# Kernel optimization log

Hardware: AMD Instinct MI355X
Metric: run time of the kernel (lower is better)

## Reference

```python
import jax, jax.numpy as jnp
import numpy as np

ASSIGN_RATIO = 0.1  # hard-coded inside coarsen_graph in the original
EPS_CUT = 1e-7
EPS_NORM = 1e-12  # torch F.normalize eps


def _normalize_batch_adj(adj):
    # adj: [B, N, N]
    n = adj.shape[1]
    A = adj + jnp.eye(n, dtype=adj.dtype)
    deg_inv_sqrt = jnp.clip(A.sum(-1), 1.0, None) ** -0.5  # [B, N]
    newA = deg_inv_sqrt[..., :, None] * A * deg_inv_sqrt[..., None, :]
    row_mask = (adj.sum(-1) > 0).astype(adj.dtype)  # [B, N]
    return row_mask[..., :, None] * newA


def setup_inputs():
    key = jax.random.key(0)
    k0, k1, k2, k3, k4 = jax.random.split(key, 5)
    B, N, D, T = 512, 128, 256, 512
    concept_hidden = jax.random.normal(k0, (B, N, D), jnp.float32)
    adj = jax.random.uniform(k1, (B, N, N), jnp.float32)
    head = jax.random.randint(k2, (B, T), 0, N)
    lin_w = jax.random.normal(k3, (1, D), jnp.float32) / np.sqrt(D).astype(np.float32)
    bias = jax.random.normal(k4, (1,), jnp.float32)
    return {"concept_hidden": concept_hidden, "adj": adj, "head": head,
            "lin_w": lin_w, "bias": bias}


def reference(concept_hidden, adj, head, lin_w, bias):
    # concept_hidden: [B, N, D], adj: [B, N, N], head: [B, T] node indices
    x = concept_hidden
    B, N, D = x.shape

    out = x @ lin_w.T                      # [B, N, 1]  self.lin(x)
    norm_adj = _normalize_batch_adj(adj)   # [B, N, N]
    out = norm_adj @ out + bias            # [B, N, 1]
    alpha = jax.nn.sigmoid(out ** 2)[..., 0]  # [B, N]

    # batch_num_nodes[i] = len(set(head[i]))  -> count unique via sort
    hs = jnp.sort(head, axis=-1)
    n_uniq = 1 + (hs[:, 1:] != hs[:, :-1]).sum(-1)  # [B]

    # per-sample k = ceil(n * 0.1) + 1 (only when n > 1); cut = k-th largest alpha
    k = jnp.ceil(n_uniq.astype(jnp.float32) * ASSIGN_RATIO).astype(jnp.int32) + 1
    a_desc = jnp.sort(alpha, axis=-1)[:, ::-1]       # descending
    idx = jnp.clip(k - 1, 0, N - 1)
    cut = jnp.take_along_axis(a_desc, idx[:, None], axis=-1)[:, 0]
    cut = jnp.where(n_uniq > 1, cut, jnp.zeros_like(cut))  # [B]

    cut_alpha = jax.nn.relu(alpha + EPS_CUT - cut[:, None])  # [B, N]

    # S = norm_adj * cut_alpha broadcast over rows, then L1-normalize rows
    S = norm_adj * cut_alpha[:, None, :]
    S = S / jnp.clip(jnp.abs(S).sum(-1, keepdims=True), EPS_NORM, None)

    St = jnp.swapaxes(S, 1, 2)             # [B, N, N]
    embedding_tensor = St @ x              # S^T x   [B, N, D]
    new_adj = (St @ adj) @ S               # S^T A S [B, N, N]
    return embedding_tensor, new_adj
```

## Files before the change

### kernel.cpp

```cpp
#include <hip/hip_runtime.h>

#define Bsz 512
#define Nn  128
#define Dd  256
#define Tt  512

typedef __attribute__((ext_vector_type(8))) short short8;
typedef __attribute__((ext_vector_type(4))) float f32x4;

__device__ __forceinline__ ushort f2bf(float f) {
    union { float f; unsigned u; } v; v.f = f;
    unsigned r = v.u + 0x7fffu + ((v.u >> 16) & 1u);
    return (ushort)(r >> 16);
}
__device__ __forceinline__ unsigned pk2(float a, float b) {
    return (unsigned)f2bf(a) | ((unsigned)f2bf(b) << 16);
}
__device__ __forceinline__ float bf2f(ushort u) {
    union { unsigned u; float f; } v; v.u = (unsigned)u << 16; return v.f;
}

__device__ __forceinline__ ushort* AP(ushort* base, int row, int col) {
    return base + row * 128 + (((col >> 3) ^ (row & 7)) << 3) + (col & 7);
}
__device__ __forceinline__ uint* XP(uint* base, int row, int col) {
    return base + row * 64 + (((col >> 2) ^ (row & 7)) << 2) + (col & 3);
}

__global__ __launch_bounds__(1024, 4) void mega(
    const float* __restrict__ x, const float* __restrict__ adj,
    const int* __restrict__ head, const float* __restrict__ lin_w,
    const float* __restrict__ bias,
    float* __restrict__ emb, float* __restrict__ nadj)
{
    const int t = threadIdx.x, b = blockIdx.x;
    __shared__ __align__(16) ushort adjR[Nn * 128];
    __shared__ __align__(16) ushort stR[Nn * 128];
    __shared__ __align__(16) uint   xtR0[Nn * 64];
    __shared__ __align__(16) uint   xtR1[Nn * 64];
    __shared__ float ttS[Nn], disS[Nn], maskS[Nn], alphaS[Nn], rowcS[Nn];
    __shared__ float partS[Nn][18];
    __shared__ float partS2[Nn][4];
    __shared__ int   flags[Nn];
    __shared__ int   nuniq;
    __shared__ float cutS;

    const float bias0 = bias[0];
    if (t < Nn) flags[t] = 0;
    if (t == 0) { nuniq = 0; cutS = 0.f; }

    const int lane = t & 63, w = t >> 6;
    const int l15 = lane & 15, quad = lane >> 4;
    const int mrow  = (w & 7) * 16;
    const int nhalf = (w >> 3) * 64;
    const int r = t >> 3, seg = t & 7;
    const int xrow = t & 127, kq0 = t >> 7;
    const float wv0 = lin_w[xrow], wv1 = lin_w[128 + xrow];

    int hv = 0;
    if (t < Tt) hv = head[(size_t)b * Tt + t];

    float e0[8], g0[8], e1[8], g1[8];
    {
        const float* xb = x + (size_t)b * Nn * Dd + xrow;
#pragma unroll
        for (int k = 0; k < 8; ++k) e0[k] = xb[(size_t)(8 * kq0 + k) * Dd];
#pragma unroll
        for (int k = 0; k < 8; ++k) g0[k] = xb[(size_t)(64 + 8 * kq0 + k) * Dd];
#pragma unroll
        for (int k = 0; k < 8; ++k) e1[k] = xb[(size_t)(8 * kq0 + k) * Dd + 128];
#pragma unroll
        for (int k = 0; k < 8; ++k) g1[k] = xb[(size_t)(64 + 8 * kq0 + k) * Dd + 128];
    }
    float4 av0, av1, av2, av3;
    {
        const float4* adjb = (const float4*)(adj + (size_t)b * Nn * Nn);
        av0 = adjb[t]; av1 = adjb[t + 1024]; av2 = adjb[t + 2048]; av3 = adjb[t + 3072];
    }

#pragma unroll
    for (int k = 0; k < 8; ++k) {
        float re = e0[k] * wv0 + e1[k] * wv1;
        float rg = g0[k] * wv0 + g1[k] * wv1;
        re += __shfl_xor(re, 1); re += __shfl_xor(re, 2); re += __shfl_xor(re, 4);
        rg += __shfl_xor(rg, 1); rg += __shfl_xor(rg, 2); rg += __shfl_xor(rg, 4);
        if ((lane & 7) == 0) {
            int gc = (w & 1) * 8 + (lane >> 3);
            partS[8 * kq0 + k][gc]      = re;
            partS[64 + 8 * kq0 + k][gc] = rg;
        }
    }

    {
        float s0 = av0.x + av0.y + av0.z + av0.w;
        float s1 = av1.x + av1.y + av1.z + av1.w;
        float s2 = av2.x + av2.y + av2.z + av2.w;
        float s3 = av3.x + av3.y + av3.z + av3.w;
        s0 += __shfl_xor(s0, 1); s0 += __shfl_xor(s0, 2); s0 += __shfl_xor(s0, 4);
        s1 += __shfl_xor(s1, 1); s1 += __shfl_xor(s1, 2); s1 += __shfl_xor(s1, 4);
        s2 += __shfl_xor(s2, 1); s2 += __shfl_xor(s2, 2); s2 += __shfl_xor(s2, 4);
        s3 += __shfl_xor(s3, 1); s3 += __shfl_xor(s3, 2); s3 += __shfl_xor(s3, 4);
        if ((lane & 7) == 0) {
            int q = (lane & 31) >> 3;
            int row0 = t >> 5;
            partS2[row0][q]       = s0;
            partS2[row0 + 32][q]  = s1;
            partS2[row0 + 64][q]  = s2;
            partS2[row0 + 96][q]  = s3;
        }
    }

    {
        uint4 q;
        q.x = pk2(e0[0], e0[1]); q.y = pk2(e0[2], e0[3]);
        q.z = pk2(e0[4], e0[5]); q.w = pk2(e0[6], e0[7]);
        *(uint4*)XP(xtR0, xrow, 4 * kq0) = q;
        q.x = pk2(g0[0], g0[1]); q.y = pk2(g0[2], g0[3]);
        q.z = pk2(g0[4], g0[5]); q.w = pk2(g0[6], g0[7]);
        *(uint4*)XP(xtR0, xrow, 4 * kq0 + 32) = q;
        q.x = pk2(e1[0], e1[1]); q.y = pk2(e1[2], e1[3]);
        q.z = pk2(e1[4], e1[5]); q.w = pk2(e1[6], e1[7]);
        *(uint4*)XP(xtR1, xrow, 4 * kq0) = q;
        q.x = pk2(g1[0], g1[1]); q.y = pk2(g1[2], g1[3]);
        q.z = pk2(g1[4], g1[5]); q.w = pk2(g1[6], g1[7]);
        *(uint4*)XP(xtR1, xrow, 4 * kq0 + 32) = q;
    }
    {
        float4 v; int f, rr2, c; uint2 w2;
        v = av0; f = t;        rr2 = f >> 5; c = (f & 31) * 4; w2.x = pk2(v.x, v.y); w2.y = pk2(v.z, v.w); *(uint2*)AP(adjR, rr2, c) = w2;
        v = av1; f = t + 1024; rr2 = f >> 5; c = (f & 31) * 4; w2.x = pk2(v.x, v.y); w2.y = pk2(v.z, v.w); *(uint2*)AP(adjR, rr2, c) = w2;
        v = av2; f = t + 2048; rr2 = f >> 5; c = (f & 31) * 4; w2.x = pk2(v.x, v.y); w2.y = pk2(v.z, v.w); *(uint2*)AP(adjR, rr2, c) = w2;
        v = av3; f = t + 3072; rr2 = f >> 5; c = (f & 31) * 4; w2.x = pk2(v.x, v.y); w2.y = pk2(v.z, v.w); *(uint2*)AP(adjR, rr2, c) = w2;
    }
    __syncthreads();

    if (t < Tt) flags[hv] = 1;

    {
        float d = partS[r][2 * seg] + partS[r][2 * seg + 1];
        float s = (seg < 4) ? partS2[r][seg] : 0.f;
        d += __shfl_xor(d, 1); d += __shfl_xor(d, 2); d += __shfl_xor(d, 4);
        s += __shfl_xor(s, 1); s += __shfl_xor(s, 2); s += __shfl_xor(s, 4);
        if (seg == 0) {
            maskS[r] = (s > 0.f) ? 1.f : 0.f;
            float dis = 1.f / sqrtf(fmaxf(s + 1.f, 1.f));
            disS[r] = dis;
            ttS[r]  = dis * d;
        }
    }
    __syncthreads();

    {
        short8 a0 = *(const short8*)AP(adjR, r, seg * 16);
        short8 a1 = *(const short8*)AP(adjR, r, seg * 16 + 8);
        f32x4 t0 = *(const f32x4*)&ttS[seg * 16];
        f32x4 t1 = *(const f32x4*)&ttS[seg * 16 + 4];
        f32x4 t2 = *(const f32x4*)&ttS[seg * 16 + 8];
        f32x4 t3 = *(const f32x4*)&ttS[seg * 16 + 12];
        float s = 0.f;
#pragma unroll
        for (int j = 0; j < 4; ++j) {
            s += bf2f((ushort)a0[j])     * t0[j];
            s += bf2f((ushort)a0[4 + j]) * t1[j];
            s += bf2f((ushort)a1[j])     * t2[j];
            s += bf2f((ushort)a1[4 + j]) * t3[j];
        }
        s += __shfl_xor(s, 1); s += __shfl_xor(s, 2); s += __shfl_xor(s, 4);
        if (seg == 0) {
            float o = maskS[r] * disS[r] * (s + ttS[r]) + bias0;
            alphaS[r] = 1.f / (1.f + expf(-o * o));
            atomicAdd(&nuniq, flags[r]);
        }
    }
    __syncthreads();

    {
        int nu = nuniq;
        if (nu > 1) {
            float an = alphaS[r];
            int cg = 0, ce = 0;
#pragma unroll
            for (int v = 0; v < 4; ++v) {
                f32x4 A = *(const f32x4*)&alphaS[seg * 16 + 4 * v];
#pragma unroll
                for (int j = 0; j < 4; ++j) { cg += (A[j] > an); ce += (A[j] == an); }
            }
            cg += __shfl_xor(cg, 1); cg += __shfl_xor(cg, 2); cg += __shfl_xor(cg, 4);
            ce += __shfl_xor(ce, 1); ce += __shfl_xor(ce, 2); ce += __shfl_xor(ce, 4);
            if (seg == 0) {
                int idx = (int)ceilf((float)nu * 0.1f);
                if (idx > Nn - 1) idx = Nn - 1;
                if (cg <= idx && idx < cg + ce) cutS = an;
            }
        }
    }
    __syncthreads();

    {
        const float cut = cutS;
        short8 a0 = *(const short8*)AP(adjR, r, seg * 16);
        short8 a1 = *(const short8*)AP(adjR, r, seg * 16 + 8);
        float s = 0.f;
#pragma unroll
        for (int v = 0; v < 4; ++v) {
            f32x4 A = *(const f32x4*)&alphaS[seg * 16 + 4 * v];
            f32x4 D = *(const f32x4*)&disS[seg * 16 + 4 * v];
#pragma unroll
            for (int j = 0; j < 4; ++j) {
                float u = fmaxf(A[j] + 1e-7f - cut, 0.f) * D[j];
                float av = (v < 2) ? bf2f((ushort)a0[4 * v + j])
                                   : bf2f((ushort)a1[4 * (v - 2) + j]);
                s += av * u;
            }
        }
        s += __shfl_xor(s, 1); s += __shfl_xor(s, 2); s += __shfl_xor(s, 4);
        if (seg == 0) {
            float ur   = fmaxf(alphaS[r] + 1e-7f - cut, 0.f) * disS[r];
            float rsum = maskS[r] * disS[r] * (ur + s);
            rowcS[r]   = maskS[r] * disS[r] / fmaxf(rsum, 1e-12f);
        }
    }
    __syncthreads();

    {
        const float cut = cutS;
        const int m = t & 127, sl = t >> 7, k0 = sl * 16;
        const float um = fmaxf(alphaS[m] + 1e-7f - cut, 0.f) * disS[m];
        float vv[16];
#pragma unroll
        for (int j = 0; j < 16; ++j) {
            int k = k0 + j;
            vv[j] = rowcS[k] * (bf2f(*AP(adjR, k, m)) + ((k == m) ? 1.f : 0.f)) * um;
        }
        uint4 p0, p1;
        p0.x = pk2(vv[0],  vv[1]);  p0.y = pk2(vv[2],  vv[3]);
        p0.z = pk2(vv[4],  vv[5]);  p0.w = pk2(vv[6],  vv[7]);
        p1.x = pk2(vv[8],  vv[9]);  p1.y = pk2(vv[10], vv[11]);
        p1.z = pk2(vv[12], vv[13]); p1.w = pk2(vv[14], vv[15]);
        *(uint4*)AP(stR, m, k0)     = p0;
        *(uint4*)AP(stR, m, k0 + 8) = p1;
    }
    __syncthreads();

    f32x4 acc[4];
#pragma unroll
    for (int nt = 0; nt < 4; ++nt) acc[nt] = (f32x4){0.f, 0.f, 0.f, 0.f};
#pragma unroll
    for (int k0 = 0; k0 < 128; k0 += 32) {
        short8 a0 = *(const short8*)AP(adjR, mrow + l15, k0 + quad * 8);
#pragma unroll
        for (int nt = 0; nt < 4; ++nt) {
            short8 bf = *(const short8*)AP(stR, nhalf + nt * 16 + l15, k0 + quad * 8);
            acc[nt] = __builtin_amdgcn_mfma_f32_16x16x32_bf16(a0, bf, acc[nt], 0, 0, 0);
        }
    }
    __syncthreads();

#pragma unroll
    for (int nt = 0; nt < 4; ++nt) {
        int j    = nhalf + nt * 16 + l15;
        int mcol = mrow + quad * 4;
        uint2 w2;
        w2.x = pk2(acc[nt][0], acc[nt][1]);
        w2.y = pk2(acc[nt][2], acc[nt][3]);
        *(uint2*)AP(adjR, j, mcol) = w2;
    }
    __syncthreads();

#pragma unroll
    for (int nt = 0; nt < 4; ++nt) acc[nt] = (f32x4){0.f, 0.f, 0.f, 0.f};
#pragma unroll
    for (int k0 = 0; k0 < 128; k0 += 32) {
        short8 a0 = *(const short8*)AP(stR, mrow + l15, k0 + quad * 8);
#pragma unroll
        for (int nt = 0; nt < 4; ++nt) {
            short8 bf = *(const short8*)AP(adjR, nhalf + nt * 16 + l15, k0 + quad * 8);
            acc[nt] = __builtin_amdgcn_mfma_f32_16x16x32_bf16(a0, bf, acc[nt], 0, 0, 0);
        }
    }
#pragma unroll
    for (int nt = 0; nt < 4; ++nt)
#pragma unroll
        for (int rr2 = 0; rr2 < 4; ++rr2) {
            int row = mrow + quad * 4 + rr2;
            int col = nhalf + nt * 16 + l15;
            nadj[((size_t)b * Nn + row) * Nn + col] = acc[nt][rr2];
        }

    const int dcb = (w >> 3) * 64;
    f32x4 accE[4];
#pragma unroll
    for (int nt = 0; nt < 4; ++nt) accE[nt] = (f32x4){0.f, 0.f, 0.f, 0.f};
#pragma unroll
    for (int ks = 0; ks < 4; ++ks) {
        short8 aE = *(const short8*)AP(stR, mrow + l15, ks * 32 + quad * 8);
#pragma unroll
        for (int nt = 0; nt < 4; ++nt) {
            short8 bf = *(const short8*)XP(xtR0, dcb + nt * 16 + l15, ks * 16 + quad * 4);
            accE[nt] = __builtin_amdgcn_mfma_f32_16x16x32_bf16(aE, bf, accE[nt], 0, 0, 0);
        }
    }
#pragma unroll
    for (int nt = 0; nt < 4; ++nt)
#pragma unroll
        for (int rr2 = 0; rr2 < 4; ++rr2) {
            int row = mrow + quad * 4 + rr2;
            int col = dcb + nt * 16 + l15;
            emb[((size_t)b * Nn + row) * Dd + col] = accE[nt][rr2];
        }

#pragma unroll
    for (int nt = 0; nt < 4; ++nt) accE[nt] = (f32x4){0.f, 0.f, 0.f, 0.f};
#pragma unroll
    for (int ks = 0; ks < 4; ++ks) {
        short8 aE = *(const short8*)AP(stR, mrow + l15, ks * 32 + quad * 8);
#pragma unroll
        for (int nt = 0; nt < 4; ++nt) {
            short8 bf = *(const short8*)XP(xtR1, dcb + nt * 16 + l15, ks * 16 + quad * 4);
            accE[nt] = __builtin_amdgcn_mfma_f32_16x16x32_bf16(aE, bf, accE[nt], 0, 0, 0);
        }
    }
#pragma unroll
    for (int nt = 0; nt < 4; ++nt)
#pragma unroll
        for (int rr2 = 0; rr2 < 4; ++rr2) {
            int row = mrow + quad * 4 + rr2;
            int col = 128 + dcb + nt * 16 + l15;
            emb[((size_t)b * Nn + row) * Dd + col] = accE[nt][rr2];
        }
}

extern "C" void kernel_launch(void* const* d_in, const int* in_sizes, int n_in,
                              void* d_out, int out_size, void* d_ws, size_t ws_size,
                              hipStream_t stream)
{
    const float* x     = (const float*)d_in[0];
    const float* adj   = (const float*)d_in[1];
    const int*   head  = (const int*)d_in[2];
    const float* lin_w = (const float*)d_in[3];
    const float* bias  = (const float*)d_in[4];

    float* emb  = (float*)d_out;
    float* nadj = emb + (size_t)Bsz * Nn * Dd;

    mega<<<Bsz, 1024, 0, stream>>>(x, adj, head, lin_w, bias, emb, nadj);
}
```

Baseline: 201.1 us.

## Split megakernel into scalar-chain kernel and GEMM kernel via workspace

```diff
diff --git a/kernel.cpp b/kernel.cpp
--- a/kernel.cpp
+++ b/kernel.cpp
@@ -27,10 +27,158 @@
     return base + row * 64 + (((col >> 2) ^ (row & 7)) << 2) + (col & 3);
 }
 
-__global__ __launch_bounds__(1024, 4) void mega(
+__global__ __launch_bounds__(256, 2) void chainK(
     const float* __restrict__ x, const float* __restrict__ adj,
     const int* __restrict__ head, const float* __restrict__ lin_w,
     const float* __restrict__ bias,
+    float* __restrict__ uws, float* __restrict__ rws)
+{
+    const int t = threadIdx.x, b = blockIdx.x;
+    __shared__ __align__(16) uint raw[8192];
+    __shared__ float dotS[Nn], ttS[Nn], disS[Nn], maskS[Nn], alphaS[Nn];
+    __shared__ int   flags[Nn];
+    __shared__ int   nuniq;
+    __shared__ float cutS;
+
+    float*  partx = (float*)raw;
+    ushort* adjB  = (ushort*)raw;
+
+    const float bias0 = bias[0];
+    if (t < Nn) flags[t] = 0;
+    if (t == 0) { nuniq = 0; cutS = 0.f; }
+    const int hv0 = head[(size_t)b * Tt + t];
+    const int hv1 = head[(size_t)b * Tt + 256 + t];
+
+    {
+        const int rep = t >> 6, d4 = t & 63;
+        const float4 w4 = ((const float4*)lin_w)[d4];
+        const float* xb = x + (size_t)b * Nn * Dd + 4 * d4;
+#pragma unroll
+        for (int i = 0; i < 32; ++i) {
+            int k = rep * 32 + i;
+            float4 v = *(const float4*)(xb + (size_t)k * Dd);
+            float p = v.x * w4.x + v.y * w4.y + v.z * w4.z + v.w * w4.w;
+            int gs = (d4 >> 2) ^ (k & 7);
+            partx[k * 64 + (gs << 2) + (d4 & 3)] = p;
+        }
+    }
+    __syncthreads();
+    {
+        const int k = t >> 1, h = t & 1;
+        float s = 0.f;
+#pragma unroll
+        for (int jj = 0; jj < 8; ++jj) {
+            int Gs = (h * 8 + jj) ^ (k & 7);
+            f32x4 q = *(const f32x4*)&partx[k * 64 + 4 * Gs];
+            s += q[0] + q[1] + q[2] + q[3];
+        }
+        s += __shfl_xor(s, 1);
+        if (h == 0) dotS[k] = s;
+        flags[hv0] = 1; flags[hv1] = 1;
+    }
+    __syncthreads();
+    {
+        const float* adjb = adj + (size_t)b * Nn * Nn;
+#pragma unroll
+        for (int i = 0; i < 16; ++i) {
+            int f = t + 256 * i;
+            int rr = f >> 5, c = (f & 31) * 4;
+            float4 v = *(const float4*)&adjb[(size_t)rr * Nn + c];
+            uint2 w2; w2.x = pk2(v.x, v.y); w2.y = pk2(v.z, v.w);
+            *(uint2*)AP(adjB, rr, c) = w2;
+        }
+    }
+    __syncthreads();
+
+    const int row = t >> 1, h = t & 1;
+    {
+        float s = 0.f;
+#pragma unroll
+        for (int j = 0; j < 8; ++j) {
+            short8 a = *(const short8*)AP(adjB, row, h * 64 + j * 8);
+#pragma unroll
+            for (int jj = 0; jj < 8; ++jj) s += bf2f((ushort)a[jj]);
+        }
+        s += __shfl_xor(s, 1);
+        if (h == 0) {
+            maskS[row] = (s > 0.f) ? 1.f : 0.f;
+            float dis = 1.f / sqrtf(fmaxf(s + 1.f, 1.f));
+            disS[row] = dis;
+            ttS[row]  = dis * dotS[row];
+        }
+    }
+    __syncthreads();
+    {
+        float s = 0.f;
+#pragma unroll
+        for (int j = 0; j < 8; ++j) {
+            short8 a = *(const short8*)AP(adjB, row, h * 64 + j * 8);
+            f32x4 t0 = *(const f32x4*)&ttS[h * 64 + j * 8];
+            f32x4 t1 = *(const f32x4*)&ttS[h * 64 + j * 8 + 4];
+#pragma unroll
+            for (int jj = 0; jj < 4; ++jj) {
+                s += bf2f((ushort)a[jj])     * t0[jj];
+                s += bf2f((ushort)a[4 + jj]) * t1[jj];
+            }
+        }
+        s += __shfl_xor(s, 1);
+        if (h == 0) {
+            float o = maskS[row] * disS[row] * (s + ttS[row]) + bias0;
+            alphaS[row] = 1.f / (1.f + expf(-o * o));
+            atomicAdd(&nuniq, flags[row]);
+        }
+    }
+    __syncthreads();
+    {
+        int nu = nuniq;
+        if (nu > 1) {
+            float an = alphaS[row];
+            int cg = 0, ce = 0;
+#pragma unroll
+            for (int v = 0; v < 16; ++v) {
+                f32x4 A = *(const f32x4*)&alphaS[h * 64 + 4 * v];
+#pragma unroll
+                for (int jj = 0; jj < 4; ++jj) { cg += (A[jj] > an); ce += (A[jj] == an); }
+            }
+            cg += __shfl_xor(cg, 1);
+            ce += __shfl_xor(ce, 1);
+            if (h == 0) {
+                int idx = (int)ceilf((float)nu * 0.1f);
+                if (idx > Nn - 1) idx = Nn - 1;
+                if (cg <= idx && idx < cg + ce) cutS = an;
+            }
+        }
+    }
+    __syncthreads();
+    {
+        const float cut = cutS;
+        float s = 0.f;
+#pragma unroll
+        for (int j = 0; j < 8; ++j) {
+            short8 a = *(const short8*)AP(adjB, row, h * 64 + j * 8);
+            f32x4 A0 = *(const f32x4*)&alphaS[h * 64 + j * 8];
+            f32x4 A1 = *(const f32x4*)&alphaS[h * 64 + j * 8 + 4];
+            f32x4 D0 = *(const f32x4*)&disS[h * 64 + j * 8];
+            f32x4 D1 = *(const f32x4*)&disS[h * 64 + j * 8 + 4];
+#pragma unroll
+            for (int jj = 0; jj < 4; ++jj) {
+                s += bf2f((ushort)a[jj])     * fmaxf(A0[jj] + 1e-7f - cut, 0.f) * D0[jj];
+                s += bf2f((ushort)a[4 + jj]) * fmaxf(A1[jj] + 1e-7f - cut, 0.f) * D1[jj];
+            }
+        }
+        s += __shfl_xor(s, 1);
+        if (h == 0) {
+            float ur   = fmaxf(alphaS[row] + 1e-7f - cut, 0.f) * disS[row];
+            float rsum = maskS[row] * disS[row] * (ur + s);
+            rws[(size_t)b * Nn + row] = maskS[row] * disS[row] / fmaxf(rsum, 1e-12f);
+            uws[(size_t)b * Nn + row] = ur;
+        }
+    }
+}
+
+__global__ __launch_bounds__(1024, 4) void gemmK(
+    const float* __restrict__ x, const float* __restrict__ adj,
+    const float* __restrict__ uws, const float* __restrict__ rws,
     float* __restrict__ emb, float* __restrict__ nadj)
 {
     const int t = threadIdx.x, b = blockIdx.x;
@@ -38,27 +186,16 @@
     __shared__ __align__(16) ushort stR[Nn * 128];
     __shared__ __align__(16) uint   xtR0[Nn * 64];
     __shared__ __align__(16) uint   xtR1[Nn * 64];
-    __shared__ float ttS[Nn], disS[Nn], maskS[Nn], alphaS[Nn], rowcS[Nn];
-    __shared__ float partS[Nn][18];
-    __shared__ float partS2[Nn][4];
-    __shared__ int   flags[Nn];
-    __shared__ int   nuniq;
-    __shared__ float cutS;
-
-    const float bias0 = bias[0];
-    if (t < Nn) flags[t] = 0;
-    if (t == 0) { nuniq = 0; cutS = 0.f; }
+    __shared__ float uS[Nn], rowcS[Nn];
 
     const int lane = t & 63, w = t >> 6;
     const int l15 = lane & 15, quad = lane >> 4;
     const int mrow  = (w & 7) * 16;
     const int nhalf = (w >> 3) * 64;
-    const int r = t >> 3, seg = t & 7;
     const int xrow = t & 127, kq0 = t >> 7;
-    const float wv0 = lin_w[xrow], wv1 = lin_w[128 + xrow];
-
-    int hv = 0;
-    if (t < Tt) hv = head[(size_t)b * Tt + t];
+
+    float uv = 0.f, rv = 0.f;
+    if (t < Nn) { uv = uws[(size_t)b * Nn + t]; rv = rws[(size_t)b * Nn + t]; }
 
     float e0[8], g0[8], e1[8], g1[8];
     {
@@ -77,39 +214,6 @@
         const float4* adjb = (const float4*)(adj + (size_t)b * Nn * Nn);
         av0 = adjb[t]; av1 = adjb[t + 1024]; av2 = adjb[t + 2048]; av3 = adjb[t + 3072];
     }
-
-#pragma unroll
-    for (int k = 0; k < 8; ++k) {
-        float re = e0[k] * wv0 + e1[k] * wv1;
-        float rg = g0[k] * wv0 + g1[k] * wv1;
-        re += __shfl_xor(re, 1); re += __shfl_xor(re, 2); re += __shfl_xor(re, 4);
-        rg += __shfl_xor(rg, 1); rg += __shfl_xor(rg, 2); rg += __shfl_xor(rg, 4);
-        if ((lane & 7) == 0) {
-            int gc = (w & 1) * 8 + (lane >> 3);
-            partS[8 * kq0 + k][gc]      = re;
-            partS[64 + 8 * kq0 + k][gc] = rg;
-        }
-    }
-
-    {
-        float s0 = av0.x + av0.y + av0.z + av0.w;
-        float s1 = av1.x + av1.y + av1.z + av1.w;
-        float s2 = av2.x + av2.y + av2.z + av2.w;
-        float s3 = av3.x + av3.y + av3.z + av3.w;
-        s0 += __shfl_xor(s0, 1); s0 += __shfl_xor(s0, 2); s0 += __shfl_xor(s0, 4);
-        s1 += __shfl_xor(s1, 1); s1 += __shfl_xor(s1, 2); s1 += __shfl_xor(s1, 4);
-        s2 += __shfl_xor(s2, 1); s2 += __shfl_xor(s2, 2); s2 += __shfl_xor(s2, 4);
-        s3 += __shfl_xor(s3, 1); s3 += __shfl_xor(s3, 2); s3 += __shfl_xor(s3, 4);
-        if ((lane & 7) == 0) {
-            int q = (lane & 31) >> 3;
-            int row0 = t >> 5;
-            partS2[row0][q]       = s0;
-            partS2[row0 + 32][q]  = s1;
-            partS2[row0 + 64][q]  = s2;
-            partS2[row0 + 96][q]  = s3;
-        }
-    }
-
     {
         uint4 q;
         q.x = pk2(e0[0], e0[1]); q.y = pk2(e0[2], e0[3]);
@@ -132,100 +236,12 @@
         v = av2; f = t + 2048; rr2 = f >> 5; c = (f & 31) * 4; w2.x = pk2(v.x, v.y); w2.y = pk2(v.z, v.w); *(uint2*)AP(adjR, rr2, c) = w2;
         v = av3; f = t + 3072; rr2 = f >> 5; c = (f & 31) * 4; w2.x = pk2(v.x, v.y); w2.y = pk2(v.z, v.w); *(uint2*)AP(adjR, rr2, c) = w2;
     }
-    __syncthreads();
-
-    if (t < Tt) flags[hv] = 1;
-
-    {
-        float d = partS[r][2 * seg] + partS[r][2 * seg + 1];
-        float s = (seg < 4) ? partS2[r][seg] : 0.f;
-        d += __shfl_xor(d, 1); d += __shfl_xor(d, 2); d += __shfl_xor(d, 4);
-        s += __shfl_xor(s, 1); s += __shfl_xor(s, 2); s += __shfl_xor(s, 4);
-        if (seg == 0) {
-            maskS[r] = (s > 0.f) ? 1.f : 0.f;
-            float dis = 1.f / sqrtf(fmaxf(s + 1.f, 1.f));
-            disS[r] = dis;
-            ttS[r]  = dis * d;
-        }
-    }
-    __syncthreads();
-
-    {
-        short8 a0 = *(const short8*)AP(adjR, r, seg * 16);
-        short8 a1 = *(const short8*)AP(adjR, r, seg * 16 + 8);
-        f32x4 t0 = *(const f32x4*)&ttS[seg * 16];
-        f32x4 t1 = *(const f32x4*)&ttS[seg * 16 + 4];
-        f32x4 t2 = *(const f32x4*)&ttS[seg * 16 + 8];
-        f32x4 t3 = *(const f32x4*)&ttS[seg * 16 + 12];
-        float s = 0.f;
-#pragma unroll
-        for (int j = 0; j < 4; ++j) {
-            s += bf2f((ushort)a0[j])     * t0[j];
-            s += bf2f((ushort)a0[4 + j]) * t1[j];
-            s += bf2f((ushort)a1[j])     * t2[j];
-            s += bf2f((ushort)a1[4 + j]) * t3[j];
-        }
-        s += __shfl_xor(s, 1); s += __shfl_xor(s, 2); s += __shfl_xor(s, 4);
-        if (seg == 0) {
-            float o = maskS[r] * disS[r] * (s + ttS[r]) + bias0;
-            alphaS[r] = 1.f / (1.f + expf(-o * o));
-            atomicAdd(&nuniq, flags[r]);
-        }
-    }
-    __syncthreads();
-
-    {
-        int nu = nuniq;
-        if (nu > 1) {
-            float an = alphaS[r];
-            int cg = 0, ce = 0;
-#pragma unroll
-            for (int v = 0; v < 4; ++v) {
-                f32x4 A = *(const f32x4*)&alphaS[seg * 16 + 4 * v];
-#pragma unroll
-                for (int j = 0; j < 4; ++j) { cg += (A[j] > an); ce += (A[j] == an); }
-            }
-            cg += __shfl_xor(cg, 1); cg += __shfl_xor(cg, 2); cg += __shfl_xor(cg, 4);
-            ce += __shfl_xor(ce, 1); ce += __shfl_xor(ce, 2); ce += __shfl_xor(ce, 4);
-            if (seg == 0) {
-                int idx = (int)ceilf((float)nu * 0.1f);
-                if (idx > Nn - 1) idx = Nn - 1;
-                if (cg <= idx && idx < cg + ce) cutS = an;
-            }
-        }
-    }
-    __syncthreads();
-
-    {
-        const float cut = cutS;
-        short8 a0 = *(const short8*)AP(adjR, r, seg * 16);
-        short8 a1 = *(const short8*)AP(adjR, r, seg * 16 + 8);
-        float s = 0.f;
-#pragma unroll
-        for (int v = 0; v < 4; ++v) {
-            f32x4 A = *(const f32x4*)&alphaS[seg * 16 + 4 * v];
-            f32x4 D = *(const f32x4*)&disS[seg * 16 + 4 * v];
-#pragma unroll
-            for (int j = 0; j < 4; ++j) {
-                float u = fmaxf(A[j] + 1e-7f - cut, 0.f) * D[j];
-                float av = (v < 2) ? bf2f((ushort)a0[4 * v + j])
-                                   : bf2f((ushort)a1[4 * (v - 2) + j]);
-                s += av * u;
-            }
-        }
-        s += __shfl_xor(s, 1); s += __shfl_xor(s, 2); s += __shfl_xor(s, 4);
-        if (seg == 0) {
-            float ur   = fmaxf(alphaS[r] + 1e-7f - cut, 0.f) * disS[r];
-            float rsum = maskS[r] * disS[r] * (ur + s);
-            rowcS[r]   = maskS[r] * disS[r] / fmaxf(rsum, 1e-12f);
-        }
-    }
-    __syncthreads();
-
-    {
-        const float cut = cutS;
+    if (t < Nn) { uS[t] = uv; rowcS[t] = rv; }
+    __syncthreads();
+
+    {
         const int m = t & 127, sl = t >> 7, k0 = sl * 16;
-        const float um = fmaxf(alphaS[m] + 1e-7f - cut, 0.f) * disS[m];
+        const float um = uS[m];
         float vv[16];
 #pragma unroll
         for (int j = 0; j < 16; ++j) {
@@ -343,5 +359,9 @@
     float* emb  = (float*)d_out;
     float* nadj = emb + (size_t)Bsz * Nn * Dd;
 
-    mega<<<Bsz, 1024, 0, stream>>>(x, adj, head, lin_w, bias, emb, nadj);
-}
+    float* uws = (float*)d_ws;
+    float* rws = uws + (size_t)Bsz * Nn;
+
+    chainK<<<Bsz, 256, 0, stream>>>(x, adj, head, lin_w, bias, uws, rws);
+    gemmK<<<Bsz, 1024, 0, stream>>>(x, adj, uws, rws, emb, nadj);
+}
```

New measurement: 209.7 us. 1.04x slower.
